# Optimization experiments

Hardware: AMD Instinct MI355X
Metric: run time of the kernel (lower is better)

The kernel has to match this reference:

```python
import jax, jax.numpy as jnp
import numpy as np

D_MODEL = 1024
N_HEADS = 16
D_HEAD = D_MODEL // N_HEADS
SEQ = 2048
BATCH = 2


def setup_inputs() -> dict:
    key = jax.random.key(0)
    ks = jax.random.split(key, 9)
    s = 1.0 / np.sqrt(D_MODEL)
    inp = {
        "x": jax.random.normal(ks[0], (BATCH, SEQ, D_MODEL), dtype=jnp.float32),
        "Wq": jax.random.uniform(ks[1], (D_MODEL, D_MODEL), jnp.float32, -s, s),
        "bq": jax.random.uniform(ks[2], (D_MODEL,), jnp.float32, -s, s),
        "Wk": jax.random.uniform(ks[3], (D_MODEL, D_MODEL), jnp.float32, -s, s),
        "bk": jax.random.uniform(ks[4], (D_MODEL,), jnp.float32, -s, s),
        "Wv": jax.random.uniform(ks[5], (D_MODEL, D_MODEL), jnp.float32, -s, s),
        "bv": jax.random.uniform(ks[6], (D_MODEL,), jnp.float32, -s, s),
        "Wo": jax.random.uniform(ks[7], (D_MODEL, D_MODEL), jnp.float32, -s, s),
        "bo": jax.random.uniform(ks[8], (D_MODEL,), jnp.float32, -s, s),
    }
    return inp


def reference(x, Wq, bq, Wk, bk, Wv, bv, Wo, bo):
    B, S, D = x.shape
    H, Dh = N_HEADS, D_HEAD
    # QKV projections (nn.Linear: x @ W.T + b; here W stored as [in, out])
    q = (x @ Wq + bq).reshape(B, S, H, Dh).transpose(0, 2, 1, 3)  # [B,H,S,Dh]
    k = (x @ Wk + bk).reshape(B, S, H, Dh).transpose(0, 2, 1, 3)
    v = (x @ Wv + bv).reshape(B, S, H, Dh).transpose(0, 2, 1, 3)
    scores = jnp.einsum("bhqd,bhkd->bhqk", q, k) / jnp.sqrt(jnp.float32(Dh))
    causal = jnp.tril(jnp.ones((S, S), dtype=bool))  # [S,S]
    scores = jnp.where(causal[None, None], scores, jnp.float32(-jnp.inf))
    attn = jax.nn.softmax(scores, axis=-1)
    # dropout is identity in eval mode
    h = jnp.einsum("bhqk,bhkd->bhqd", attn, v)  # [B,H,S,Dh]
    h = h.transpose(0, 2, 1, 3).reshape(B, S, D)
    return h @ Wo + bo
```

## Files before the change

kernel.cpp:

```cpp
#include <hip/hip_runtime.h>

typedef unsigned short u16;
typedef unsigned int u32;
typedef __attribute__((ext_vector_type(8))) __bf16 bf16x8;
typedef __attribute__((ext_vector_type(4))) float f32x4;
typedef __attribute__((ext_vector_type(4))) unsigned short u16x4;
typedef __attribute__((ext_vector_type(2))) unsigned int u32x2;

#define SEQ 2048
#define DM 1024
#define NH 16
#define DH 64

__device__ __forceinline__ float fexp2(float x) {
  return __builtin_amdgcn_exp2f(x);
}

__device__ __forceinline__ unsigned short f2bf(float f) {
  unsigned u = __builtin_bit_cast(unsigned, f);
  u += 0x7fffu + ((u >> 16) & 1u);
  return (unsigned short)(u >> 16);
}

__device__ __forceinline__ u32 cvtpk(float lo, float hi) {
  u32 r;
  asm("v_cvt_pk_bf16_f32 %0, %1, %2" : "=v"(r) : "v"(lo), "v"(hi));
  return r;
}

__device__ __forceinline__ void gload_lds16(const u16* g, u16* l) {
  __builtin_amdgcn_global_load_lds(
      (const __attribute__((address_space(1))) u16*)g,
      (__attribute__((address_space(3))) u16*)l, 16, 0, 0);
}

__global__ __launch_bounds__(256) void cvt_kernel(const float* __restrict__ in,
                                                  u16* __restrict__ out, int n4) {
  int id = blockIdx.x * 256 + threadIdx.x;
  if (id >= n4) return;
  float4 v = ((const float4*)in)[id];
  u16x4 o = { f2bf(v.x), f2bf(v.y), f2bf(v.z), f2bf(v.w) };
  ((u16x4*)out)[id] = o;
}

__global__ __launch_bounds__(256) void wtrans_kernel(const float* __restrict__ W0,
                                                     const float* __restrict__ W1,
                                                     const float* __restrict__ W2,
                                                     const float* __restrict__ W3,
                                                     u16* __restrict__ WtBase) {
  const float* W = (blockIdx.z == 0) ? W0 : (blockIdx.z == 1) ? W1
                 : (blockIdx.z == 2) ? W2 : W3;
  u16* Wt = WtBase + ((size_t)blockIdx.z << 20);
  __shared__ float tile[32][33];
  int tx = threadIdx.x & 31, ty = threadIdx.x >> 5;
  int k0 = blockIdx.y * 32, n0 = blockIdx.x * 32;
#pragma unroll
  for (int j = 0; j < 32; j += 8)
    tile[ty + j][tx] = W[(size_t)(k0 + ty + j) * DM + n0 + tx];
  __syncthreads();
#pragma unroll
  for (int j = 0; j < 32; j += 8)
    Wt[(size_t)(n0 + ty + j) * DM + k0 + tx] = f2bf(tile[tx][ty + j]);
}

template <int BM, int BN>
__global__ __launch_bounds__(256) void gemm_kernel(
    const u16* __restrict__ A, const u16* __restrict__ WtBase,
    const float* __restrict__ b0, const float* __restrict__ b1,
    const float* __restrict__ b2,
    void* __restrict__ O0, void* __restrict__ O1, void* __restrict__ O2,
    int modeBase) {
  constexpr int MR = BM / 32, NR = BN / 32;
  const int Kd = 1024, Nd = 1024;
  const int mode = modeBase + blockIdx.z;
  const u16* Bt = WtBase + ((size_t)blockIdx.z << 20);
  const float* bias = (blockIdx.z == 0) ? b0 : (blockIdx.z == 1) ? b1 : b2;
  void* Out = (blockIdx.z == 0) ? O0 : (blockIdx.z == 1) ? O1 : O2;

  __shared__ u16 As[2][BM * 64];
  __shared__ u16 Bs[2][BN * 64];
  const int tid = threadIdx.x;
  const int lane = tid & 63, w = tid >> 6;
  const int lrow = lane & 15, u = lane >> 4;
  const int wr = w >> 1, wc = w & 1;
  const int brow = blockIdx.y * BM, bcol = blockIdx.x * BN;

  f32x4 acc[MR][NR] = {};

  auto stage = [&](int kt, int buf) {
#pragma unroll
    for (int i = 0; i < BM / 32; ++i) {
      const int p = i * 4096 + tid * 16;
      const int row = p >> 7;
      const int chunk = ((p >> 4) & 7) ^ (row & 7);
      gload_lds16(A + (size_t)(brow + row) * Kd + kt + chunk * 8, As[buf] + (p >> 1));
    }
#pragma unroll
    for (int i = 0; i < BN / 32; ++i) {
      const int p = i * 4096 + tid * 16;
      const int row = p >> 7;
      const int chunk = ((p >> 4) & 7) ^ (row & 7);
      gload_lds16(Bt + (size_t)(bcol + row) * Kd + kt + chunk * 8, Bs[buf] + (p >> 1));
    }
  };

  stage(0, 0);
  __syncthreads();

  for (int it = 0; it < 16; ++it) {
    const int cur = it & 1;
    if (it + 1 < 16) stage((it + 1) * 64, cur ^ 1);
#pragma unroll
    for (int ks = 0; ks < 2; ++ks) {
      const int c = ks * 64 + u * 16;
      bf16x8 af[MR], bfr[NR];
#pragma unroll
      for (int m = 0; m < MR; ++m) {
        const int r = wr * (BM / 2) + m * 16 + lrow;
        af[m] = *(const bf16x8*)(As[cur] + ((r * 128 + (c ^ ((r & 7) << 4))) >> 1));
      }
#pragma unroll
      for (int n = 0; n < NR; ++n) {
        const int r = wc * (BN / 2) + n * 16 + lrow;
        bfr[n] = *(const bf16x8*)(Bs[cur] + ((r * 128 + (c ^ ((r & 7) << 4))) >> 1));
      }
#pragma unroll
      for (int m = 0; m < MR; ++m)
#pragma unroll
        for (int n = 0; n < NR; ++n)
          acc[m][n] = __builtin_amdgcn_mfma_f32_16x16x32_bf16(af[m], bfr[n], acc[m][n], 0, 0, 0);
    }
    __syncthreads();
  }

  const int r0 = brow + wr * (BM / 2) + u * 4;
  const int c0 = bcol + wc * (BN / 2) + lrow;
#pragma unroll
  for (int m = 0; m < MR; ++m) {
#pragma unroll
    for (int n = 0; n < NR; ++n) {
      const int col = c0 + n * 16;
      const float bv = bias[col];
      if (mode == 3) {
        float* O = (float*)Out;
#pragma unroll
        for (int i = 0; i < 4; ++i) {
          int row = r0 + m * 16 + i;
          O[(size_t)row * Nd + col] = acc[m][n][i] + bv;
        }
      } else if (mode == 2) {
        const int rowb = r0 + m * 16;
        const int b = rowb >> 11, s = rowb & 2047;
        const int h = col >> 6, dh = col & 63;
        u16x4 pk;
#pragma unroll
        for (int i = 0; i < 4; ++i) pk[i] = f2bf(acc[m][n][i] + bv);
        u16* O = (u16*)Out;
        *(u16x4*)(O + ((size_t)((b * NH + h) * DH + dh) * SEQ + s)) = pk;
      } else {
        const float sc = (mode == 0) ? 0.1803368801111204f : 1.0f;
        u16* O = (u16*)Out;
#pragma unroll
        for (int i = 0; i < 4; ++i) {
          int row = r0 + m * 16 + i;
          int b = row >> 11, s = row & 2047;
          int h = col >> 6, dh = col & 63;
          O[((size_t)(b * NH + h) * SEQ + s) * DH + dh] = f2bf((acc[m][n][i] + bv) * sc);
        }
      }
    }
  }
}

__device__ __forceinline__ void softmax_update(f32x4 (&s)[4], f32x4 (&hacc)[4],
                                               float& m_i, float& l_i) {
  float pg0 = fmaxf(fmaxf(s[0][0], s[0][1]), fmaxf(s[0][2], s[0][3]));
  float pg1 = fmaxf(fmaxf(s[1][0], s[1][1]), fmaxf(s[1][2], s[1][3]));
  float pg2 = fmaxf(fmaxf(s[2][0], s[2][1]), fmaxf(s[2][2], s[2][3]));
  float pg3 = fmaxf(fmaxf(s[3][0], s[3][1]), fmaxf(s[3][2], s[3][3]));
  float pmax = fmaxf(fmaxf(pg0, pg1), fmaxf(pg2, pg3));
  pmax = fmaxf(pmax, __shfl_xor(pmax, 16));
  pmax = fmaxf(pmax, __shfl_xor(pmax, 32));
  if (__any(pmax > m_i + 8.0f)) {
    const float mnew = fmaxf(m_i, pmax);
    const float scl = fexp2(m_i - mnew);
    l_i *= scl;
#pragma unroll
    for (int g = 0; g < 4; ++g) hacc[g] *= scl;
    m_i = mnew;
  }
  float rs = 0.f;
#pragma unroll
  for (int g = 0; g < 4; ++g)
#pragma unroll
    for (int i = 0; i < 4; ++i) {
      const float p = fexp2(s[g][i] - m_i);
      s[g][i] = p;
      rs += p;
    }
  rs += __shfl_xor(rs, 16);
  rs += __shfl_xor(rs, 32);
  l_i += rs;
}

__device__ __forceinline__ void write_p(u16* ps, const f32x4 (&s)[4], int lrow, int u) {
#pragma unroll
  for (int g = 0; g < 4; ++g) {
    u32x2 pw = { cvtpk(s[g][0], s[g][1]), cvtpk(s[g][2], s[g][3]) };
    *(u32x2*)(ps + ((lrow * 128 + ((g * 32 + u * 8) ^ ((lrow & 7) << 4))) >> 1)) = pw;
  }
}

__global__ __launch_bounds__(256, 2) void attn_kernel(const u16* __restrict__ Qb,
                                                      const u16* __restrict__ Kb,
                                                      const u16* __restrict__ Vt,
                                                      u16* __restrict__ Hh) {
  const int px = blockIdx.x, bh = blockIdx.y;
  const int qtA = px, qtB = 31 - px;
  const int tid = threadIdx.x, lane = tid & 63, w = tid >> 6;
  const int lrow = lane & 15, u = lane >> 4;

  const u16* Qp = Qb + (size_t)bh * SEQ * DH;
  const u16* Kp = Kb + (size_t)bh * SEQ * DH;
  const u16* Vp = Vt + (size_t)bh * DH * SEQ;

  __shared__ u16 KV[2][2][4096];
  __shared__ u16 Ps[4][2][1024];

  const int q0A = qtA * 64 + w * 16, q0B = qtB * 64 + w * 16;
  bf16x8 qfA[2], qfB[2];
#pragma unroll
  for (int ks = 0; ks < 2; ++ks) {
    qfA[ks] = *(const bf16x8*)(Qp + (size_t)(q0A + lrow) * DH + ks * 32 + u * 8);
    qfB[ks] = *(const bf16x8*)(Qp + (size_t)(q0B + lrow) * DH + ks * 32 + u * 8);
  }

  float mA = -1e30f, lA = 0.f, mB = -1e30f, lB = 0.f;
  f32x4 haccA[4], haccB[4];
#pragma unroll
  for (int g = 0; g < 4; ++g) {
    haccA[g] = (f32x4){0.f, 0.f, 0.f, 0.f};
    haccB[g] = (f32x4){0.f, 0.f, 0.f, 0.f};
  }

  auto stage = [&](int kt, int buf) {
#pragma unroll
    for (int i = 0; i < 2; ++i) {
      const int p = i * 4096 + tid * 16;
      const int row = p >> 7;
      const int c16 = ((p >> 4) & 7) ^ (row & 7);
      gload_lds16(Kp + (size_t)(kt * 64 + row) * 64 + c16 * 8, &KV[buf][0][p >> 1]);
      gload_lds16(Vp + (size_t)row * 2048 + (size_t)kt * 64 + c16 * 8, &KV[buf][1][p >> 1]);
    }
  };

  stage(0, 0);
  __syncthreads();

  const int wq = w * 16 + lrow;
  const int nkt = qtB + 1;
  for (int kt = 0; kt < nkt; ++kt) {
    const int cur = kt & 1;
    if (kt + 1 < nkt) stage(kt + 1, cur ^ 1);
    const u16* bufK = KV[cur][0];
    const u16* bufV = KV[cur][1];
    const bool doA = (kt <= qtA);

    bf16x8 kf[2][4];
#pragma unroll
    for (int ks = 0; ks < 2; ++ks) {
      const int c = ks * 64 + u * 16;
#pragma unroll
      for (int g = 0; g < 4; ++g) {
        const int r = g * 16 + lrow;
        kf[ks][g] = *(const bf16x8*)(bufK + ((r * 128 + (c ^ ((r & 7) << 4))) >> 1));
      }
    }
    f32x4 sA[4] = {}, sB[4] = {};
#pragma unroll
    for (int ks = 0; ks < 2; ++ks)
#pragma unroll
      for (int g = 0; g < 4; ++g)
        sB[g] = __builtin_amdgcn_mfma_f32_16x16x32_bf16(kf[ks][g], qfB[ks], sB[g], 0, 0, 0);
    if (doA) {
#pragma unroll
      for (int ks = 0; ks < 2; ++ks)
#pragma unroll
        for (int g = 0; g < 4; ++g)
          sA[g] = __builtin_amdgcn_mfma_f32_16x16x32_bf16(kf[ks][g], qfA[ks], sA[g], 0, 0, 0);
    }
    if (kt == qtB) {
#pragma unroll
      for (int g = 0; g < 4; ++g) {
        const int kb = g * 16 + u * 4;
#pragma unroll
        for (int i = 0; i < 4; ++i)
          if (kb + i > wq) sB[g][i] = -1e30f;
      }
    }
    softmax_update(sB, haccB, mB, lB);
    write_p(&Ps[w][1][0], sB, lrow, u);
    if (doA) {
      if (kt == qtA) {
#pragma unroll
        for (int g = 0; g < 4; ++g) {
          const int kb = g * 16 + u * 4;
#pragma unroll
          for (int i = 0; i < 4; ++i)
            if (kb + i > wq) sA[g][i] = -1e30f;
        }
      }
      softmax_update(sA, haccA, mA, lA);
      write_p(&Ps[w][0][0], sA, lrow, u);
    }
    bf16x8 vf[2][4], pfB[2], pfA[2];
#pragma unroll
    for (int ks = 0; ks < 2; ++ks) {
      const int c = ks * 64 + u * 16;
#pragma unroll
      for (int g = 0; g < 4; ++g) {
        const int r = g * 16 + lrow;
        vf[ks][g] = *(const bf16x8*)(bufV + ((r * 128 + (c ^ ((r & 7) << 4))) >> 1));
      }
      pfB[ks] = *(const bf16x8*)(&Ps[w][1][0] + ((lrow * 128 + (c ^ ((lrow & 7) << 4))) >> 1));
      if (doA)
        pfA[ks] = *(const bf16x8*)(&Ps[w][0][0] + ((lrow * 128 + (c ^ ((lrow & 7) << 4))) >> 1));
    }
#pragma unroll
    for (int ks = 0; ks < 2; ++ks)
#pragma unroll
      for (int g = 0; g < 4; ++g)
        haccB[g] = __builtin_amdgcn_mfma_f32_16x16x32_bf16(vf[ks][g], pfB[ks], haccB[g], 0, 0, 0);
    if (doA) {
#pragma unroll
      for (int ks = 0; ks < 2; ++ks)
#pragma unroll
        for (int g = 0; g < 4; ++g)
          haccA[g] = __builtin_amdgcn_mfma_f32_16x16x32_bf16(vf[ks][g], pfA[ks], haccA[g], 0, 0, 0);
    }
    __syncthreads();
  }

  const int b = bh >> 4, h = bh & 15;
  {
    const float inv = 1.0f / lA;
    u16* dst = Hh + ((size_t)b * SEQ + (q0A + lrow)) * DM + h * DH + u * 4;
#pragma unroll
    for (int g = 0; g < 4; ++g) {
      u32x2 pk = { cvtpk(haccA[g][0] * inv, haccA[g][1] * inv),
                   cvtpk(haccA[g][2] * inv, haccA[g][3] * inv) };
      *(u32x2*)(dst + g * 16) = pk;
    }
  }
  {
    const float inv = 1.0f / lB;
    u16* dst = Hh + ((size_t)b * SEQ + (q0B + lrow)) * DM + h * DH + u * 4;
#pragma unroll
    for (int g = 0; g < 4; ++g) {
      u32x2 pk = { cvtpk(haccB[g][0] * inv, haccB[g][1] * inv),
                   cvtpk(haccB[g][2] * inv, haccB[g][3] * inv) };
      *(u32x2*)(dst + g * 16) = pk;
    }
  }
}

extern "C" void kernel_launch(void* const* d_in, const int* in_sizes, int n_in,
                              void* d_out, int out_size, void* d_ws, size_t ws_size,
                              hipStream_t stream) {
  const float* x  = (const float*)d_in[0];
  const float* Wq = (const float*)d_in[1];
  const float* bq = (const float*)d_in[2];
  const float* Wk = (const float*)d_in[3];
  const float* bk = (const float*)d_in[4];
  const float* Wv = (const float*)d_in[5];
  const float* bv = (const float*)d_in[6];
  const float* Wo = (const float*)d_in[7];
  const float* bo = (const float*)d_in[8];
  float* out = (float*)d_out;

  char* ws = (char*)d_ws;
  u16* Xb  = (u16*)(ws);
  u16* Wt  = (u16*)(ws + (8u << 20));
  u16* Qb  = (u16*)(ws + (16u << 20));
  u16* Kb  = (u16*)(ws + (24u << 20));
  u16* Vt  = (u16*)(ws + (32u << 20));
  u16* Hh  = (u16*)(ws + (40u << 20));
  (void)in_sizes; (void)n_in; (void)out_size; (void)ws_size;

  cvt_kernel<<<4096, 256, 0, stream>>>(x, Xb, 4096 * 1024 / 4);
  dim3 tg(32, 32, 4);
  wtrans_kernel<<<tg, 256, 0, stream>>>(Wq, Wk, Wv, Wo, Wt);
  dim3 gq(8, 32, 3);
  gemm_kernel<128, 128><<<gq, 256, 0, stream>>>(Xb, Wt, bq, bk, bv, Qb, Kb, Vt, 0);
  dim3 ga(16, 32);
  attn_kernel<<<ga, 256, 0, stream>>>(Qb, Kb, Vt, Hh);
  dim3 go(16, 32, 1);
  gemm_kernel<128, 64><<<go, 256, 0, stream>>>(Hh, Wt + (3u << 20), bo, bo, bo, out, out, out, 3);
}
```

Before: 207.6 us.

## Merge prep kernels and shrink GEMM K-tile to raise occupancy

Merges the x-to-bf16 conversion and the weight transpose into one launch, with a fifth z-slice of blocks doing the conversion. Halves the GEMM K-tile from 64 to 32, which halves shared memory per block and adds a launch-bounds hint of 4 blocks per CU so more waves can be resident. The trade-off is twice as many main-loop iterations and barriers per tile, with less MFMA work between syncs. The swizzle is adjusted to the narrower 64-byte rows.

```diff
diff --git a/kernel.cpp b/kernel.cpp
--- a/kernel.cpp
+++ b/kernel.cpp
@@ -34,20 +34,24 @@
       (__attribute__((address_space(3))) u16*)l, 16, 0, 0);
 }
 
-__global__ __launch_bounds__(256) void cvt_kernel(const float* __restrict__ in,
-                                                  u16* __restrict__ out, int n4) {
-  int id = blockIdx.x * 256 + threadIdx.x;
-  if (id >= n4) return;
-  float4 v = ((const float4*)in)[id];
-  u16x4 o = { f2bf(v.x), f2bf(v.y), f2bf(v.z), f2bf(v.w) };
-  ((u16x4*)out)[id] = o;
-}
-
-__global__ __launch_bounds__(256) void wtrans_kernel(const float* __restrict__ W0,
-                                                     const float* __restrict__ W1,
-                                                     const float* __restrict__ W2,
-                                                     const float* __restrict__ W3,
-                                                     u16* __restrict__ WtBase) {
+__global__ __launch_bounds__(256) void prep_kernel(const float* __restrict__ x,
+                                                   const float* __restrict__ W0,
+                                                   const float* __restrict__ W1,
+                                                   const float* __restrict__ W2,
+                                                   const float* __restrict__ W3,
+                                                   u16* __restrict__ WtBase,
+                                                   u16* __restrict__ Xb) {
+  if (blockIdx.z == 4) {
+    const int id = (blockIdx.y * 32 + blockIdx.x) * 256 + threadIdx.x;
+#pragma unroll
+    for (int rep = 0; rep < 4; ++rep) {
+      const int idx = rep * 262144 + id;
+      float4 v = ((const float4*)x)[idx];
+      u16x4 o = { f2bf(v.x), f2bf(v.y), f2bf(v.z), f2bf(v.w) };
+      ((u16x4*)Xb)[idx] = o;
+    }
+    return;
+  }
   const float* W = (blockIdx.z == 0) ? W0 : (blockIdx.z == 1) ? W1
                  : (blockIdx.z == 2) ? W2 : W3;
   u16* Wt = WtBase + ((size_t)blockIdx.z << 20);
@@ -64,7 +68,7 @@
 }
 
 template <int BM, int BN>
-__global__ __launch_bounds__(256) void gemm_kernel(
+__global__ __launch_bounds__(256, 4) void gemm_kernel(
     const u16* __restrict__ A, const u16* __restrict__ WtBase,
     const float* __restrict__ b0, const float* __restrict__ b1,
     const float* __restrict__ b2,
@@ -77,8 +81,8 @@
   const float* bias = (blockIdx.z == 0) ? b0 : (blockIdx.z == 1) ? b1 : b2;
   void* Out = (blockIdx.z == 0) ? O0 : (blockIdx.z == 1) ? O1 : O2;
 
-  __shared__ u16 As[2][BM * 64];
-  __shared__ u16 Bs[2][BN * 64];
+  __shared__ u16 As[2][BM * 32];
+  __shared__ u16 Bs[2][BN * 32];
   const int tid = threadIdx.x;
   const int lane = tid & 63, w = tid >> 6;
   const int lrow = lane & 15, u = lane >> 4;
@@ -89,17 +93,17 @@
 
   auto stage = [&](int kt, int buf) {
 #pragma unroll
-    for (int i = 0; i < BM / 32; ++i) {
+    for (int i = 0; i < BM / 64; ++i) {
       const int p = i * 4096 + tid * 16;
-      const int row = p >> 7;
-      const int chunk = ((p >> 4) & 7) ^ (row & 7);
+      const int row = p >> 6;
+      const int chunk = ((p >> 4) & 3) ^ (row & 3);
       gload_lds16(A + (size_t)(brow + row) * Kd + kt + chunk * 8, As[buf] + (p >> 1));
     }
 #pragma unroll
-    for (int i = 0; i < BN / 32; ++i) {
+    for (int i = 0; i < BN / 64; ++i) {
       const int p = i * 4096 + tid * 16;
-      const int row = p >> 7;
-      const int chunk = ((p >> 4) & 7) ^ (row & 7);
+      const int row = p >> 6;
+      const int chunk = ((p >> 4) & 3) ^ (row & 3);
       gload_lds16(Bt + (size_t)(bcol + row) * Kd + kt + chunk * 8, Bs[buf] + (p >> 1));
     }
   };
@@ -107,29 +111,25 @@
   stage(0, 0);
   __syncthreads();
 
-  for (int it = 0; it < 16; ++it) {
+  for (int it = 0; it < 32; ++it) {
     const int cur = it & 1;
-    if (it + 1 < 16) stage((it + 1) * 64, cur ^ 1);
-#pragma unroll
-    for (int ks = 0; ks < 2; ++ks) {
-      const int c = ks * 64 + u * 16;
-      bf16x8 af[MR], bfr[NR];
-#pragma unroll
-      for (int m = 0; m < MR; ++m) {
-        const int r = wr * (BM / 2) + m * 16 + lrow;
-        af[m] = *(const bf16x8*)(As[cur] + ((r * 128 + (c ^ ((r & 7) << 4))) >> 1));
-      }
-#pragma unroll
-      for (int n = 0; n < NR; ++n) {
-        const int r = wc * (BN / 2) + n * 16 + lrow;
-        bfr[n] = *(const bf16x8*)(Bs[cur] + ((r * 128 + (c ^ ((r & 7) << 4))) >> 1));
-      }
-#pragma unroll
-      for (int m = 0; m < MR; ++m)
-#pragma unroll
-        for (int n = 0; n < NR; ++n)
-          acc[m][n] = __builtin_amdgcn_mfma_f32_16x16x32_bf16(af[m], bfr[n], acc[m][n], 0, 0, 0);
-    }
+    if (it + 1 < 32) stage((it + 1) * 32, cur ^ 1);
+    bf16x8 af[MR], bfr[NR];
+#pragma unroll
+    for (int m = 0; m < MR; ++m) {
+      const int r = wr * (BM / 2) + m * 16 + lrow;
+      af[m] = *(const bf16x8*)(As[cur] + ((r * 64 + ((u * 16) ^ ((r & 3) << 4))) >> 1));
+    }
+#pragma unroll
+    for (int n = 0; n < NR; ++n) {
+      const int r = wc * (BN / 2) + n * 16 + lrow;
+      bfr[n] = *(const bf16x8*)(Bs[cur] + ((r * 64 + ((u * 16) ^ ((r & 3) << 4))) >> 1));
+    }
+#pragma unroll
+    for (int m = 0; m < MR; ++m)
+#pragma unroll
+      for (int n = 0; n < NR; ++n)
+        acc[m][n] = __builtin_amdgcn_mfma_f32_16x16x32_bf16(af[m], bfr[n], acc[m][n], 0, 0, 0);
     __syncthreads();
   }
 
@@ -387,9 +387,8 @@
   u16* Hh  = (u16*)(ws + (40u << 20));
   (void)in_sizes; (void)n_in; (void)out_size; (void)ws_size;
 
-  cvt_kernel<<<4096, 256, 0, stream>>>(x, Xb, 4096 * 1024 / 4);
-  dim3 tg(32, 32, 4);
-  wtrans_kernel<<<tg, 256, 0, stream>>>(Wq, Wk, Wv, Wo, Wt);
+  dim3 tp(32, 32, 5);
+  prep_kernel<<<tp, 256, 0, stream>>>(x, Wq, Wk, Wv, Wo, Wt, Xb);
   dim3 gq(8, 32, 3);
   gemm_kernel<128, 128><<<gq, 256, 0, stream>>>(Xb, Wt, bq, bk, bv, Qb, Kb, Vt, 0);
   dim3 ga(16, 32);
```

After: 194.5 us. -6.3%, faster.
